# Kernel tuning notes

Hardware: AMD Instinct MI355X
Metric: run time of the kernel (lower is better)

## Reference

```python
import jax, jax.numpy as jnp
import numpy as np

N_NODES = 100000
N_EDGES = 1600000
N_GRAPHS = 256
HIDDEN = 128
IN_FEAT = 5


def setup_inputs() -> dict:
    key = jax.random.key(0)
    ks = jax.random.split(key, 12)
    x = jax.random.normal(ks[0], (N_NODES, IN_FEAT), dtype=jnp.float32)
    edge_index = jax.random.randint(ks[1], (2, N_EDGES), 0, N_NODES, dtype=jnp.int64)
    batch = jnp.sort(jax.random.randint(ks[2], (N_NODES,), 0, N_GRAPHS, dtype=jnp.int64))
    s = 0.05
    W0 = jax.random.normal(ks[3], (IN_FEAT, HIDDEN), dtype=jnp.float32) * s
    b0 = jnp.zeros((HIDDEN,), dtype=jnp.float32)
    W1 = jax.random.normal(ks[4], (HIDDEN, HIDDEN), dtype=jnp.float32) * s
    b1 = jnp.zeros((HIDDEN,), dtype=jnp.float32)
    W2 = jax.random.normal(ks[5], (HIDDEN, HIDDEN), dtype=jnp.float32) * s
    b2 = jnp.zeros((HIDDEN,), dtype=jnp.float32)
    lin_w = jax.random.normal(ks[6], (HIDDEN, 1), dtype=jnp.float32) * s
    lin_b = jnp.zeros((1,), dtype=jnp.float32)
    return {"x": x, "edge_index": edge_index, "batch": batch,
            "W0": W0, "b0": b0, "W1": W1, "b1": b1, "W2": W2, "b2": b2,
            "lin_w": lin_w, "lin_b": lin_b}


def reference(x, edge_index, batch, W0, b0, W1, b1, W2, b2, lin_w, lin_b):
    n = x.shape[0]
    # PyG GCNConv: add self-loops, symmetric normalization D^-1/2 (A+I) D^-1/2
    loop = jnp.arange(n, dtype=edge_index.dtype)
    src = jnp.concatenate([edge_index[0], loop])  # [E+N]
    dst = jnp.concatenate([edge_index[1], loop])
    deg = jax.ops.segment_sum(jnp.ones_like(dst, dtype=x.dtype), dst, num_segments=n)
    dis = jnp.where(deg > 0, jax.lax.rsqrt(jnp.maximum(deg, 1.0)), 0.0)
    norm = (dis[src] * dis[dst])[:, None]  # [E+N, 1]

    def gcn_conv(h, W, b):
        h = h @ W                      # [N, H]
        msg = h[src] * norm            # gather + scale, [E+N, H]
        return jax.ops.segment_sum(msg, dst, num_segments=n) + b

    h = jax.nn.relu(gcn_conv(x, W0, b0))
    h = jax.nn.relu(gcn_conv(h, W1, b1))
    h = gcn_conv(h, W2, b2)

    # global_mean_pool over batch ids
    sums = jax.ops.segment_sum(h, batch, num_segments=N_GRAPHS)
    cnt = jax.ops.segment_sum(jnp.ones((n,), x.dtype), batch, num_segments=N_GRAPHS)
    g = sums / jnp.maximum(cnt, 1.0)[:, None]
    # dropout p=0.01 is identity in eval mode
    return jax.nn.sigmoid(g @ lin_w + lin_b)  # [N_GRAPHS, 1]
```

## Files before the change

kernel.cpp:

```cpp
#include <hip/hip_runtime.h>
#include <hip/hip_fp8.h>

#define GCN_N 100000
#define GCN_H 128
#define GCN_G 256
#define NPB_SHIFT 9
#define NPB 512
#define NBKT 196
#define CHUNK 2048
#define SRC_BITS 17
#define SRC_MASK ((1 << SRC_BITS) - 1)
#define T1_SCALE 256.0f
#define T1_INV_SCALE (1.0f / 256.0f)

static_assert(GCN_N < (1 << SRC_BITS), "src id must fit 17 bits");

using short8 = __attribute__((ext_vector_type(8))) short;
using f32x4  = __attribute__((ext_vector_type(4))) float;
using f32x2  = __attribute__((ext_vector_type(2))) float;

#if defined(__has_builtin)
#if __has_builtin(__builtin_amdgcn_cvt_pk_f32_fp8) && __has_builtin(__builtin_amdgcn_cvt_pk_fp8_f32)
#define HW_FP8 1
#endif
#endif


__device__ __forceinline__ unsigned short f2bf(float f) {
    unsigned u = __float_as_uint(f);
    unsigned r = u + 0x7FFFu + ((u >> 16) & 1u);
    return (unsigned short)(r >> 16);
}
__device__ __forceinline__ float bf2f(unsigned short h) {
    return __uint_as_float(((unsigned)h) << 16);
}

__device__ __forceinline__ void fp8x4_to_f32(unsigned v, float* f) {
#ifdef HW_FP8
    f32x2 lo = __builtin_amdgcn_cvt_pk_f32_fp8((int)v, false);
    f32x2 hi = __builtin_amdgcn_cvt_pk_f32_fp8((int)v, true);
    f[0] = lo[0]; f[1] = lo[1]; f[2] = hi[0]; f[3] = hi[1];
#else
    #pragma unroll
    for (int j = 0; j < 4; j++) {
        __hip_fp8_e4m3 h;
        h.__x = (unsigned char)((v >> (8 * j)) & 0xFF);
        f[j] = (float)h;
    }
#endif
}

__device__ __forceinline__ unsigned f32x4_to_fp8(float f0, float f1, float f2, float f3) {
#ifdef HW_FP8
    int r = __builtin_amdgcn_cvt_pk_fp8_f32(f0, f1, 0, false);
    r = __builtin_amdgcn_cvt_pk_fp8_f32(f2, f3, r, true);
    return (unsigned)r;
#else
    unsigned r = 0;
    float ff[4] = {f0, f1, f2, f3};
    #pragma unroll
    for (int j = 0; j < 4; j++) {
        __hip_fp8_e4m3 h(ff[j]);
        r |= ((unsigned)h.__x) << (8 * j);
    }
    return r;
#endif
}


__global__ __launch_bounds__(256) void hist_kernel(const int* __restrict__ dst,
                                                   int* __restrict__ hist, int E) {
    __shared__ int lh[NBKT];
    int tid = threadIdx.x;
    if (tid < NBKT) lh[tid] = 0;
    __syncthreads();
    int e0 = blockIdx.x * CHUNK;
    #pragma unroll
    for (int i = 0; i < CHUNK / 256; i++) {
        int e = e0 + tid + i * 256;
        if (e < E) atomicAdd(&lh[dst[e] >> NPB_SHIFT], 1);
    }
    __syncthreads();
    if (tid < NBKT) hist[(size_t)blockIdx.x * NBKT + tid] = lh[tid];
}

__global__ __launch_bounds__(64) void scan_cols_kernel(const int* __restrict__ hist,
                                                       int* __restrict__ offsT,
                                                       int* __restrict__ btot, int B) {
    int k = blockIdx.x;
    int lane = threadIdx.x;
    int running = 0;
    for (int b0 = 0; b0 < B; b0 += 64) {
        int b = b0 + lane;
        int v = (b < B) ? hist[(size_t)b * NBKT + k] : 0;
        int iv = v;
        #pragma unroll
        for (int d = 1; d < 64; d <<= 1) {
            int x = __shfl_up(iv, d, 64);
            if (lane >= d) iv += x;
        }
        if (b < B) offsT[(size_t)k * B + b] = running + iv - v;
        running += __shfl(iv, 63, 64);
    }
    if (lane == 0) btot[k] = running;
}

__global__ void bucket_base_kernel(const int* __restrict__ btot,
                                   int* __restrict__ bbase,
                                   int* __restrict__ rowptr, int n) {
    if (threadIdx.x == 0 && blockIdx.x == 0) {
        int run = 0;
        for (int i = 0; i < NBKT; i++) { bbase[i] = run; run += btot[i]; }
        bbase[NBKT] = run;
        rowptr[n] = run;
    }
}

__global__ __launch_bounds__(256) void partition_kernel(const int* __restrict__ src,
                                                        const int* __restrict__ dst,
                                                        const int* __restrict__ bbase,
                                                        const int* __restrict__ offsT,
                                                        int* __restrict__ epack,
                                                        int E, int B) {
    __shared__ int cur[NBKT];
    int blk = blockIdx.x, tid = threadIdx.x;
    if (tid < NBKT) cur[tid] = bbase[tid] + offsT[(size_t)tid * B + blk];
    __syncthreads();
    int e0 = blk * CHUNK;
    #pragma unroll
    for (int i = 0; i < CHUNK / 256; i++) {
        int e = e0 + tid + i * 256;
        if (e < E) {
            int d = dst[e];
            int s = src[e];
            int pos = atomicAdd(&cur[d >> NPB_SHIFT], 1);
            epack[pos] = ((d & (NPB - 1)) << SRC_BITS) | s;
        }
    }
}

__global__ __launch_bounds__(512) void csr_build_kernel(const int* __restrict__ epack,
                                                        const int* __restrict__ bbase,
                                                        int* __restrict__ rowptr,
                                                        float* __restrict__ dis,
                                                        int* __restrict__ csrc, int n) {
    __shared__ int lcount[NPB];
    __shared__ int lcur[NPB];
    __shared__ int wsums[8];
    int k = blockIdx.x, tid = threadIdx.x;
    int lane = tid & 63, wid = tid >> 6;
    int nodebase = k << NPB_SHIFT;
    int ebeg = bbase[k], eend = bbase[k + 1];

    lcount[tid] = 0;
    __syncthreads();
    for (int e = ebeg + tid; e < eend; e += 512)
        atomicAdd(&lcount[epack[e] >> SRC_BITS], 1);
    __syncthreads();

    int v = lcount[tid];
    int iv = v;
    #pragma unroll
    for (int d = 1; d < 64; d <<= 1) {
        int x = __shfl_up(iv, d, 64);
        if (lane >= d) iv += x;
    }
    if (lane == 63) wsums[wid] = iv;
    __syncthreads();
    if (tid == 0) {
        int r = 0;
        #pragma unroll
        for (int w = 0; w < 8; w++) { int t = wsums[w]; wsums[w] = r; r += t; }
    }
    __syncthreads();
    int ex = wsums[wid] + iv - v;
    lcur[tid] = ex;
    int node = nodebase + tid;
    if (node < n) {
        rowptr[node] = ebeg + ex;
        dis[node] = rsqrtf((float)(v + 1));
    }
    __syncthreads();
    for (int e = ebeg + tid; e < eend; e += 512) {
        int p = epack[e];
        int pos = atomicAdd(&lcur[p >> SRC_BITS], 1);
        csrc[ebeg + pos] = p & SRC_MASK;
    }
}


__global__ __launch_bounds__(256) void xscale_kernel(const float* __restrict__ x,
                                                     const float* __restrict__ dis,
                                                     float* __restrict__ xsp, int n) {
    int i = blockIdx.x * 256 + threadIdx.x;
    if (i >= n) return;
    float di = dis[i];
    float4 a;
    a.x = x[(size_t)i * 5 + 0] * di;
    a.y = x[(size_t)i * 5 + 1] * di;
    a.z = x[(size_t)i * 5 + 2] * di;
    a.w = x[(size_t)i * 5 + 3] * di;
    float a4 = x[(size_t)i * 5 + 4] * di;
    ((float4*)(xsp + (size_t)i * 8))[0] = a;
    xsp[(size_t)i * 8 + 4] = a4;
}

__global__ __launch_bounds__(256) void aggx_kernel(const float* __restrict__ xsp,
                                                   const float* __restrict__ dis,
                                                   const int* __restrict__ rowptr,
                                                   const int* __restrict__ csrc,
                                                   float* __restrict__ a0p, int n) {
    int i = blockIdx.x * 256 + threadIdx.x;
    if (i >= n) return;
    float4 acc = ((const float4*)(xsp + (size_t)i * 8))[0];
    float acc4 = xsp[(size_t)i * 8 + 4];
    int r0 = rowptr[i], r1 = rowptr[i + 1];
    for (int e = r0; e < r1; e++) {
        int s = csrc[e];
        float4 v = ((const float4*)(xsp + (size_t)s * 8))[0];
        acc.x += v.x; acc.y += v.y; acc.z += v.z; acc.w += v.w;
        acc4 += xsp[(size_t)s * 8 + 4];
    }
    float di = dis[i];
    acc.x *= di; acc.y *= di; acc.z *= di; acc.w *= di; acc4 *= di;
    ((float4*)(a0p + (size_t)i * 8))[0] = acc;
    a0p[(size_t)i * 8 + 4] = acc4;
}


__global__ __launch_bounds__(256) void mmfused_kernel(const float* __restrict__ a0p,
                                                      const float* __restrict__ W0,
                                                      const float* __restrict__ b0,
                                                      const float* __restrict__ W1,
                                                      const float* __restrict__ dis,
                                                      unsigned* __restrict__ t1f8, int n) {
    __shared__ __align__(16) unsigned short sA[128 * 128];
    __shared__ __align__(16) unsigned short sBT[128 * 128];
    __shared__ __align__(16) float4 sA0[256];
    __shared__ float sDis[128];
    char* sAb = (char*)sA;
    char* sBb = (char*)sBT;
    int tid = threadIdx.x;
    int rowBase = blockIdx.x * 128;

    {
        int rowL = tid >> 1, q = tid & 1;
        int gr = rowBase + rowL;
        float4 v = make_float4(0.f, 0.f, 0.f, 0.f);
        if (gr < n) v = ((const float4*)a0p)[(size_t)gr * 2 + q];
        sA0[tid] = v;
        if (tid < 128) {
            int g2 = rowBase + tid;
            sDis[tid] = (g2 < n) ? dis[g2] : 0.f;
        }
    }
    for (int idx = tid; idx < 128 * 32; idx += 256) {
        int k = idx >> 5, c4 = idx & 31;
        float4 w = ((const float4*)W1)[idx];
        int col0 = c4 * 4;
        float wv[4] = {w.x, w.y, w.z, w.w};
        #pragma unroll
        for (int j = 0; j < 4; j++) {
            int col = col0 + j;
            int byteoff = (col * 256 + k * 2) ^ ((col & 7) << 4);
            *(unsigned short*)(sBb + byteoff) = f2bf(wv[j]);
        }
    }
    __syncthreads();

    {
        int cq = tid & 31;
        int rg = tid >> 5;
        float4 w0q[5];
        #pragma unroll
        for (int j = 0; j < 5; j++) w0q[j] = *((const float4*)(W0 + j * 128 + cq * 4));
        float4 b0q = *((const float4*)(b0 + cq * 4));
        const float* sA0f = (const float*)sA0;
        #pragma unroll
        for (int ri = 0; ri < 16; ri++) {
            int row = rg + ri * 8;
            const float* ar = sA0f + row * 8;
            float4 h = b0q;
            #pragma unroll
            for (int j = 0; j < 5; j++) {
                float aj = ar[j];
                h.x = fmaf(aj, w0q[j].x, h.x);
                h.y = fmaf(aj, w0q[j].y, h.y);
                h.z = fmaf(aj, w0q[j].z, h.z);
                h.w = fmaf(aj, w0q[j].w, h.w);
            }
            h.x = fmaxf(h.x, 0.f); h.y = fmaxf(h.y, 0.f);
            h.z = fmaxf(h.z, 0.f); h.w = fmaxf(h.w, 0.f);
            uint2 p;
            p.x = (unsigned)f2bf(h.x) | ((unsigned)f2bf(h.y) << 16);
            p.y = (unsigned)f2bf(h.z) | ((unsigned)f2bf(h.w) << 16);
            int byteoff = (row * 256 + cq * 8) ^ ((row & 7) << 4);
            *(uint2*)(sAb + byteoff) = p;
        }
    }
    __syncthreads();

    int wave = tid >> 6, l = tid & 63;
    int lr = l & 15, lg = l >> 4;
    int rb = wave * 32;

    short8 afr[2][4];
    #pragma unroll
    for (int rt = 0; rt < 2; rt++) {
        int row = rb + rt * 16 + lr;
        #pragma unroll
        for (int ks = 0; ks < 4; ks++) {
            int byteoff = (row * 256 + ks * 64 + lg * 16) ^ ((row & 7) << 4);
            afr[rt][ks] = *(const short8*)(sAb + byteoff);
        }
    }
    f32x4 acc[2][8];
    #pragma unroll
    for (int rt = 0; rt < 2; rt++)
        #pragma unroll
        for (int ct = 0; ct < 8; ct++)
            acc[rt][ct] = (f32x4){0.f, 0.f, 0.f, 0.f};

    #pragma unroll
    for (int ct = 0; ct < 8; ct++) {
        int col = ct * 16 + lr;
        short8 bfr[4];
        #pragma unroll
        for (int ks = 0; ks < 4; ks++) {
            int byteoff = (col * 256 + ks * 64 + lg * 16) ^ ((col & 7) << 4);
            bfr[ks] = *(const short8*)(sBb + byteoff);
        }
        #pragma unroll
        for (int rt = 0; rt < 2; rt++) {
            #pragma unroll
            for (int ks = 0; ks < 4; ks++) {
                acc[rt][ct] = __builtin_amdgcn_mfma_f32_16x16x32_bf16(
                    afr[rt][ks], bfr[ks], acc[rt][ct], 0, 0, 0);
            }
        }
    }

    #pragma unroll
    for (int rt = 0; rt < 2; rt++) {
        #pragma unroll
        for (int i = 0; i < 4; i++) {
            int rowL = rb + rt * 16 + lg * 4 + i;
            float dsc = sDis[rowL] * T1_SCALE;
            #pragma unroll
            for (int ct = 0; ct < 8; ct++) {
                int col = ct * 16 + lr;
                int byteoff = (rowL * 256 + col * 2) ^ ((rowL & 7) << 4);
                *(unsigned short*)(sAb + byteoff) = f2bf(acc[rt][ct][i] * dsc);
            }
        }
    }
    __syncthreads();

    #pragma unroll
    for (int it = 0; it < 8; it++) {
        int flat = tid + it * 256;
        int rowL = flat >> 4, c16 = flat & 15;
        int gr = rowBase + rowL;
        if (gr < n) {
            int byteoff = (rowL * 256 + c16 * 16) ^ ((rowL & 7) << 4);
            uint4 v = *(const uint4*)(sAb + byteoff);
            float f0 = __uint_as_float(v.x << 16), f1 = __uint_as_float(v.x & 0xFFFF0000u);
            float f2 = __uint_as_float(v.y << 16), f3 = __uint_as_float(v.y & 0xFFFF0000u);
            float f4 = __uint_as_float(v.z << 16), f5 = __uint_as_float(v.z & 0xFFFF0000u);
            float f6 = __uint_as_float(v.w << 16), f7 = __uint_as_float(v.w & 0xFFFF0000u);
            uint2 p;
            p.x = f32x4_to_fp8(f0, f1, f2, f3);
            p.y = f32x4_to_fp8(f4, f5, f6, f7);
            ((uint2*)t1f8)[(size_t)gr * 16 + c16] = p;
        }
    }
}


__global__ __launch_bounds__(256) void w2l_kernel(const float* __restrict__ W2,
                                                  const float* __restrict__ b2,
                                                  const float* __restrict__ lw,
                                                  float* __restrict__ w2l,
                                                  float* __restrict__ c2) {
    __shared__ float slw[128];
    int tid = threadIdx.x;
    if (tid < 128) slw[tid] = lw[tid];
    __syncthreads();
    if (tid < 128) {
        float s = 0.f;
        #pragma unroll 8
        for (int j = 0; j < 128; j++) s = fmaf(W2[tid * 128 + j], slw[j], s);
        w2l[tid] = s;
    } else if (tid == 128) {
        float s = 0.f;
        for (int j = 0; j < 128; j++) s = fmaf(b2[j], slw[j], s);
        c2[0] = s;
    }
}


__global__ __launch_bounds__(256) void agg1_kernel(const unsigned* __restrict__ t1f8,
                                                   const float* __restrict__ dis,
                                                   const int* __restrict__ rowptr,
                                                   const int* __restrict__ csrc,
                                                   const float* __restrict__ b1,
                                                   const float* __restrict__ w2l,
                                                   float* __restrict__ z, int n) {
    int group = threadIdx.x >> 5, lane = threadIdx.x & 31;
    int i = blockIdx.x * 8 + group;
    if (i >= n) return;
    float f[4];
    unsigned sv = t1f8[(size_t)i * 32 + lane];
    fp8x4_to_f32(sv, f);
    float4 acc = make_float4(f[0], f[1], f[2], f[3]);
    int r0 = rowptr[i], r1 = rowptr[i + 1];
    int e = r0;
    for (; e + 7 < r1; e += 8) {
        unsigned vv[8];
        #pragma unroll
        for (int u = 0; u < 8; u++) vv[u] = t1f8[(size_t)csrc[e + u] * 32 + lane];
        #pragma unroll
        for (int u = 0; u < 8; u++) {
            fp8x4_to_f32(vv[u], f);
            acc.x += f[0]; acc.y += f[1]; acc.z += f[2]; acc.w += f[3];
        }
    }
    for (; e < r1; e++) {
        unsigned v = t1f8[(size_t)csrc[e] * 32 + lane];
        fp8x4_to_f32(v, f);
        acc.x += f[0]; acc.y += f[1]; acc.z += f[2]; acc.w += f[3];
    }
    float di = dis[i];
    float dis_s = di * T1_INV_SCALE;
    float4 b4 = ((const float4*)b1)[lane];
    acc.x = fmaf(dis_s, acc.x, b4.x);
    acc.y = fmaf(dis_s, acc.y, b4.y);
    acc.z = fmaf(dis_s, acc.z, b4.z);
    acc.w = fmaf(dis_s, acc.w, b4.w);
    acc.x = fmaxf(acc.x, 0.f); acc.y = fmaxf(acc.y, 0.f);
    acc.z = fmaxf(acc.z, 0.f); acc.w = fmaxf(acc.w, 0.f);
    float4 w = ((const float4*)w2l)[lane];
    float d = acc.x * w.x + acc.y * w.y + acc.z * w.z + acc.w * w.w;
    #pragma unroll
    for (int o = 16; o > 0; o >>= 1) d += __shfl_down(d, o, 32);
    if (lane == 0) z[i] = di * d;
}


__global__ __launch_bounds__(256) void aggz_kernel(const float* __restrict__ z,
                                                   const float* __restrict__ dis,
                                                   const int* __restrict__ rowptr,
                                                   const int* __restrict__ csrc,
                                                   float* __restrict__ nd, int n) {
    int i = blockIdx.x * 256 + threadIdx.x;
    if (i >= n) return;
    float acc = z[i];
    int r0 = rowptr[i], r1 = rowptr[i + 1];
    int e = r0;
    for (; e + 3 < r1; e += 4) {
        acc += (z[csrc[e]] + z[csrc[e + 1]]) + (z[csrc[e + 2]] + z[csrc[e + 3]]);
    }
    for (; e < r1; e++) acc += z[csrc[e]];
    nd[i] = dis[i] * acc;
}


__global__ __launch_bounds__(256) void boundary_kernel(const int* __restrict__ batch,
                                                       int* __restrict__ gstart, int n) {
    int i = blockIdx.x * 256 + threadIdx.x;
    if (i >= n) return;
    int b = batch[i];
    int pb = (i == 0) ? -1 : batch[i - 1];
    for (int g = pb + 1; g <= b; g++) gstart[g] = i;
    if (i == n - 1) {
        for (int g = b + 1; g <= GCN_G; g++) gstart[g] = n;
    }
}

__global__ __launch_bounds__(256) void reduce_kernel(const float* __restrict__ nd,
                                                     const int* __restrict__ gstart,
                                                     const float* __restrict__ c2,
                                                     const float* __restrict__ lb,
                                                     float* __restrict__ out) {
    __shared__ float ssum[4];
    int g = blockIdx.x;
    int s = gstart[g], epos = gstart[g + 1];
    int tid = threadIdx.x, lane = tid & 63, wid = tid >> 6;
    float sum = 0.f;
    for (int i = s + tid; i < epos; i += 256) sum += nd[i];
    #pragma unroll
    for (int o = 32; o > 0; o >>= 1) sum += __shfl_down(sum, o, 64);
    if (lane == 0) ssum[wid] = sum;
    __syncthreads();
    if (tid == 0) {
        float tot = ssum[0] + ssum[1] + ssum[2] + ssum[3];
        float cnt = (float)max(epos - s, 1);
        float v = tot / cnt + c2[0] + lb[0];
        out[g] = 1.f / (1.f + expf(-v));
    }
}


extern "C" void kernel_launch(void* const* d_in, const int* in_sizes, int n_in,
                              void* d_out, int out_size, void* d_ws, size_t ws_size,
                              hipStream_t stream) {
    const float* x   = (const float*)d_in[0];
    const int*   ei  = (const int*)d_in[1];
    const int*   bat = (const int*)d_in[2];
    const float* W0  = (const float*)d_in[3];
    const float* b0  = (const float*)d_in[4];
    const float* W1  = (const float*)d_in[5];
    const float* b1  = (const float*)d_in[6];
    const float* W2  = (const float*)d_in[7];
    const float* b2  = (const float*)d_in[8];
    const float* lw  = (const float*)d_in[9];
    const float* lb  = (const float*)d_in[10];
    float* out = (float*)d_out;

    const int N = GCN_N;
    const int E = in_sizes[1] / 2;
    const int B = (E + CHUNK - 1) / CHUNK;

    char* ws = (char*)d_ws;
    size_t off = 0;
    auto alloc = [&](size_t bytes) {
        size_t o = off;
        off += (bytes + 255) & ~(size_t)255;
        return o;
    };
    int*   hist    = (int*)(ws + alloc((size_t)B * NBKT * 4));
    int*   offsT   = (int*)(ws + alloc((size_t)NBKT * B * 4));
    int*   btot    = (int*)(ws + alloc((size_t)NBKT * 4));
    int*   bbase   = (int*)(ws + alloc((size_t)(NBKT + 1) * 4));
    int*   epack   = (int*)(ws + alloc((size_t)E * 4));
    int*   rowptr  = (int*)(ws + alloc((size_t)(N + 1) * 4));
    float* dis     = (float*)(ws + alloc((size_t)N * 4));
    int*   csrc    = (int*)(ws + alloc((size_t)E * 4));
    float* xsp     = (float*)(ws + alloc((size_t)N * 8 * 4));
    float* a0p     = (float*)(ws + alloc((size_t)N * 8 * 4));
    unsigned* t1f8 = (unsigned*)(ws + alloc((size_t)N * GCN_H));
    float* z       = (float*)(ws + alloc((size_t)N * 4));
    float* nd      = (float*)(ws + alloc((size_t)N * 4));
    int*   gstart  = (int*)(ws + alloc((size_t)(GCN_G + 1) * 4));
    float* w2l     = (float*)(ws + alloc(128 * 4));
    float* c2      = (float*)(ws + alloc(4));

    const int* src = ei;
    const int* dst = ei + E;

    hist_kernel<<<B, 256, 0, stream>>>(dst, hist, E);
    scan_cols_kernel<<<NBKT, 64, 0, stream>>>(hist, offsT, btot, B);
    bucket_base_kernel<<<1, 64, 0, stream>>>(btot, bbase, rowptr, N);
    partition_kernel<<<B, 256, 0, stream>>>(src, dst, bbase, offsT, epack, E, B);
    csr_build_kernel<<<NBKT, 512, 0, stream>>>(epack, bbase, rowptr, dis, csrc, N);
    boundary_kernel<<<(N + 255) / 256, 256, 0, stream>>>(bat, gstart, N);
    w2l_kernel<<<1, 256, 0, stream>>>(W2, b2, lw, w2l, c2);

    xscale_kernel<<<(N + 255) / 256, 256, 0, stream>>>(x, dis, xsp, N);
    aggx_kernel<<<(N + 255) / 256, 256, 0, stream>>>(xsp, dis, rowptr, csrc, a0p, N);
    mmfused_kernel<<<(N + 127) / 128, 256, 0, stream>>>(a0p, W0, b0, W1, dis, t1f8, N);
    agg1_kernel<<<N / 8, 256, 0, stream>>>(t1f8, dis, rowptr, csrc, b1, w2l, z, N);
    aggz_kernel<<<(N + 255) / 256, 256, 0, stream>>>(z, dis, rowptr, csrc, nd, N);

    reduce_kernel<<<GCN_G, 256, 0, stream>>>(nd, gstart, c2, lb, out);
}
```

Baseline: 170.8 us.

## Fuse x scaling into CSR build, pre-convert W1, fuse pooling into final aggregation

Several independent changes. The x-scaling kernel is folded into the CSR build, and W1 is converted to transposed bf16 once in a small kernel so each matmul block does vector loads instead of per-element conversion. The first aggregation is unrolled by four. agg1 now gives each node 16 lanes of 8 fp8 values each, so each block covers twice as many nodes. The last aggregation is fused with mean pooling through shared-memory and global atomics, which removes the nd buffer and the per-graph reduce kernel but adds a memset and float atomic ordering nondeterminism.

New measurement: 152.0 us. 11.0% less time.

```diff
diff --git a/kernel.cpp b/kernel.cpp
--- a/kernel.cpp
+++ b/kernel.cpp
@@ -141,8 +141,10 @@
 
 __global__ __launch_bounds__(512) void csr_build_kernel(const int* __restrict__ epack,
                                                         const int* __restrict__ bbase,
+                                                        const float* __restrict__ x,
                                                         int* __restrict__ rowptr,
                                                         float* __restrict__ dis,
+                                                        float* __restrict__ xsp,
                                                         int* __restrict__ csrc, int n) {
     __shared__ int lcount[NPB];
     __shared__ int lcur[NPB];
@@ -162,8 +164,8 @@
     int iv = v;
     #pragma unroll
     for (int d = 1; d < 64; d <<= 1) {
-        int x = __shfl_up(iv, d, 64);
-        if (lane >= d) iv += x;
+        int x2 = __shfl_up(iv, d, 64);
+        if (lane >= d) iv += x2;
     }
     if (lane == 63) wsums[wid] = iv;
     __syncthreads();
@@ -178,7 +180,17 @@
     int node = nodebase + tid;
     if (node < n) {
         rowptr[node] = ebeg + ex;
-        dis[node] = rsqrtf((float)(v + 1));
+        float dd = rsqrtf((float)(v + 1));
+        dis[node] = dd;
+        const float* xr = x + (size_t)node * 5;
+        float4 a;
+        a.x = xr[0] * dd; a.y = xr[1] * dd; a.z = xr[2] * dd; a.w = xr[3] * dd;
+        float a4 = xr[4] * dd;
+        ((float4*)(xsp + (size_t)node * 8))[0] = a;
+        xsp[(size_t)node * 8 + 4] = a4;
+        xsp[(size_t)node * 8 + 5] = 0.f;
+        xsp[(size_t)node * 8 + 6] = 0.f;
+        xsp[(size_t)node * 8 + 7] = 0.f;
     }
     __syncthreads();
     for (int e = ebeg + tid; e < eend; e += 512) {
@@ -188,22 +200,6 @@
     }
 }
 
-
-__global__ __launch_bounds__(256) void xscale_kernel(const float* __restrict__ x,
-                                                     const float* __restrict__ dis,
-                                                     float* __restrict__ xsp, int n) {
-    int i = blockIdx.x * 256 + threadIdx.x;
-    if (i >= n) return;
-    float di = dis[i];
-    float4 a;
-    a.x = x[(size_t)i * 5 + 0] * di;
-    a.y = x[(size_t)i * 5 + 1] * di;
-    a.z = x[(size_t)i * 5 + 2] * di;
-    a.w = x[(size_t)i * 5 + 3] * di;
-    float a4 = x[(size_t)i * 5 + 4] * di;
-    ((float4*)(xsp + (size_t)i * 8))[0] = a;
-    xsp[(size_t)i * 8 + 4] = a4;
-}
 
 __global__ __launch_bounds__(256) void aggx_kernel(const float* __restrict__ xsp,
                                                    const float* __restrict__ dis,
@@ -215,7 +211,24 @@
     float4 acc = ((const float4*)(xsp + (size_t)i * 8))[0];
     float acc4 = xsp[(size_t)i * 8 + 4];
     int r0 = rowptr[i], r1 = rowptr[i + 1];
-    for (int e = r0; e < r1; e++) {
+    int e = r0;
+    for (; e + 3 < r1; e += 4) {
+        int s0 = csrc[e], s1 = csrc[e + 1], s2 = csrc[e + 2], s3 = csrc[e + 3];
+        float4 v0 = ((const float4*)(xsp + (size_t)s0 * 8))[0];
+        float a40 = xsp[(size_t)s0 * 8 + 4];
+        float4 v1 = ((const float4*)(xsp + (size_t)s1 * 8))[0];
+        float a41 = xsp[(size_t)s1 * 8 + 4];
+        float4 v2 = ((const float4*)(xsp + (size_t)s2 * 8))[0];
+        float a42 = xsp[(size_t)s2 * 8 + 4];
+        float4 v3 = ((const float4*)(xsp + (size_t)s3 * 8))[0];
+        float a43 = xsp[(size_t)s3 * 8 + 4];
+        acc.x += (v0.x + v1.x) + (v2.x + v3.x);
+        acc.y += (v0.y + v1.y) + (v2.y + v3.y);
+        acc.z += (v0.z + v1.z) + (v2.z + v3.z);
+        acc.w += (v0.w + v1.w) + (v2.w + v3.w);
+        acc4  += (a40 + a41) + (a42 + a43);
+    }
+    for (; e < r1; e++) {
         int s = csrc[e];
         float4 v = ((const float4*)(xsp + (size_t)s * 8))[0];
         acc.x += v.x; acc.y += v.y; acc.z += v.z; acc.w += v.w;
@@ -228,10 +241,39 @@
 }
 
 
+__global__ __launch_bounds__(256) void w2l_kernel(const float* __restrict__ W2,
+                                                  const float* __restrict__ b2,
+                                                  const float* __restrict__ lw,
+                                                  float* __restrict__ w2l,
+                                                  float* __restrict__ c2) {
+    __shared__ float slw[128];
+    int tid = threadIdx.x;
+    if (tid < 128) slw[tid] = lw[tid];
+    __syncthreads();
+    if (tid < 128) {
+        float s = 0.f;
+        #pragma unroll 8
+        for (int j = 0; j < 128; j++) s = fmaf(W2[tid * 128 + j], slw[j], s);
+        w2l[tid] = s;
+    } else if (tid == 128) {
+        float s = 0.f;
+        for (int j = 0; j < 128; j++) s = fmaf(b2[j], slw[j], s);
+        c2[0] = s;
+    }
+}
+
+__global__ __launch_bounds__(256) void w1cvt_kernel(const float* __restrict__ W1,
+                                                    unsigned short* __restrict__ w1t) {
+    int idx = blockIdx.x * 256 + threadIdx.x;
+    int col = idx >> 7, k = idx & 127;
+    w1t[idx] = f2bf(W1[k * 128 + col]);
+}
+
+
 __global__ __launch_bounds__(256) void mmfused_kernel(const float* __restrict__ a0p,
                                                       const float* __restrict__ W0,
                                                       const float* __restrict__ b0,
-                                                      const float* __restrict__ W1,
+                                                      const unsigned short* __restrict__ w1t,
                                                       const float* __restrict__ dis,
                                                       unsigned* __restrict__ t1f8, int n) {
     __shared__ __align__(16) unsigned short sA[128 * 128];
@@ -254,17 +296,13 @@
             sDis[tid] = (g2 < n) ? dis[g2] : 0.f;
         }
     }
-    for (int idx = tid; idx < 128 * 32; idx += 256) {
-        int k = idx >> 5, c4 = idx & 31;
-        float4 w = ((const float4*)W1)[idx];
-        int col0 = c4 * 4;
-        float wv[4] = {w.x, w.y, w.z, w.w};
-        #pragma unroll
-        for (int j = 0; j < 4; j++) {
-            int col = col0 + j;
-            int byteoff = (col * 256 + k * 2) ^ ((col & 7) << 4);
-            *(unsigned short*)(sBb + byteoff) = f2bf(wv[j]);
-        }
+    #pragma unroll
+    for (int it = 0; it < 8; it++) {
+        int idx = tid + it * 256;
+        int col = idx >> 4, c = idx & 15;
+        uint4 v = ((const uint4*)w1t)[idx];
+        int byteoff = (col * 256 + c * 16) ^ ((col & 7) << 4);
+        *(uint4*)(sBb + byteoff) = v;
     }
     __syncthreads();
 
@@ -377,28 +415,6 @@
 }
 
 
-__global__ __launch_bounds__(256) void w2l_kernel(const float* __restrict__ W2,
-                                                  const float* __restrict__ b2,
-                                                  const float* __restrict__ lw,
-                                                  float* __restrict__ w2l,
-                                                  float* __restrict__ c2) {
-    __shared__ float slw[128];
-    int tid = threadIdx.x;
-    if (tid < 128) slw[tid] = lw[tid];
-    __syncthreads();
-    if (tid < 128) {
-        float s = 0.f;
-        #pragma unroll 8
-        for (int j = 0; j < 128; j++) s = fmaf(W2[tid * 128 + j], slw[j], s);
-        w2l[tid] = s;
-    } else if (tid == 128) {
-        float s = 0.f;
-        for (int j = 0; j < 128; j++) s = fmaf(b2[j], slw[j], s);
-        c2[0] = s;
-    }
-}
-
-
 __global__ __launch_bounds__(256) void agg1_kernel(const unsigned* __restrict__ t1f8,
                                                    const float* __restrict__ dis,
                                                    const int* __restrict__ rowptr,
@@ -406,62 +422,96 @@
                                                    const float* __restrict__ b1,
                                                    const float* __restrict__ w2l,
                                                    float* __restrict__ z, int n) {
-    int group = threadIdx.x >> 5, lane = threadIdx.x & 31;
-    int i = blockIdx.x * 8 + group;
+    int group = threadIdx.x >> 4, lane = threadIdx.x & 15;
+    int i = blockIdx.x * 16 + group;
     if (i >= n) return;
-    float f[4];
-    unsigned sv = t1f8[(size_t)i * 32 + lane];
-    fp8x4_to_f32(sv, f);
-    float4 acc = make_float4(f[0], f[1], f[2], f[3]);
+    const uint2* t2 = (const uint2*)t1f8;
+    float f[8];
+    uint2 sv = t2[(size_t)i * 16 + lane];
+    fp8x4_to_f32(sv.x, f);
+    fp8x4_to_f32(sv.y, f + 4);
+    float acc[8];
+    #pragma unroll
+    for (int j = 0; j < 8; j++) acc[j] = f[j];
     int r0 = rowptr[i], r1 = rowptr[i + 1];
     int e = r0;
     for (; e + 7 < r1; e += 8) {
-        unsigned vv[8];
-        #pragma unroll
-        for (int u = 0; u < 8; u++) vv[u] = t1f8[(size_t)csrc[e + u] * 32 + lane];
+        uint2 vv[8];
+        #pragma unroll
+        for (int u = 0; u < 8; u++) vv[u] = t2[(size_t)csrc[e + u] * 16 + lane];
         #pragma unroll
         for (int u = 0; u < 8; u++) {
-            fp8x4_to_f32(vv[u], f);
-            acc.x += f[0]; acc.y += f[1]; acc.z += f[2]; acc.w += f[3];
+            fp8x4_to_f32(vv[u].x, f);
+            fp8x4_to_f32(vv[u].y, f + 4);
+            #pragma unroll
+            for (int j = 0; j < 8; j++) acc[j] += f[j];
         }
     }
     for (; e < r1; e++) {
-        unsigned v = t1f8[(size_t)csrc[e] * 32 + lane];
-        fp8x4_to_f32(v, f);
-        acc.x += f[0]; acc.y += f[1]; acc.z += f[2]; acc.w += f[3];
+        uint2 v = t2[(size_t)csrc[e] * 16 + lane];
+        fp8x4_to_f32(v.x, f);
+        fp8x4_to_f32(v.y, f + 4);
+        #pragma unroll
+        for (int j = 0; j < 8; j++) acc[j] += f[j];
     }
     float di = dis[i];
     float dis_s = di * T1_INV_SCALE;
-    float4 b4 = ((const float4*)b1)[lane];
-    acc.x = fmaf(dis_s, acc.x, b4.x);
-    acc.y = fmaf(dis_s, acc.y, b4.y);
-    acc.z = fmaf(dis_s, acc.z, b4.z);
-    acc.w = fmaf(dis_s, acc.w, b4.w);
-    acc.x = fmaxf(acc.x, 0.f); acc.y = fmaxf(acc.y, 0.f);
-    acc.z = fmaxf(acc.z, 0.f); acc.w = fmaxf(acc.w, 0.f);
-    float4 w = ((const float4*)w2l)[lane];
-    float d = acc.x * w.x + acc.y * w.y + acc.z * w.z + acc.w * w.w;
-    #pragma unroll
-    for (int o = 16; o > 0; o >>= 1) d += __shfl_down(d, o, 32);
+    float4 b4a = ((const float4*)b1)[lane * 2];
+    float4 b4b = ((const float4*)b1)[lane * 2 + 1];
+    float4 w4a = ((const float4*)w2l)[lane * 2];
+    float4 w4b = ((const float4*)w2l)[lane * 2 + 1];
+    float bb[8] = {b4a.x, b4a.y, b4a.z, b4a.w, b4b.x, b4b.y, b4b.z, b4b.w};
+    float ww[8] = {w4a.x, w4a.y, w4a.z, w4a.w, w4b.x, w4b.y, w4b.z, w4b.w};
+    float d = 0.f;
+    #pragma unroll
+    for (int j = 0; j < 8; j++) {
+        float c = fmaxf(fmaf(dis_s, acc[j], bb[j]), 0.f);
+        d = fmaf(c, ww[j], d);
+    }
+    #pragma unroll
+    for (int o = 8; o > 0; o >>= 1) d += __shfl_down(d, o, 16);
     if (lane == 0) z[i] = di * d;
 }
 
 
-__global__ __launch_bounds__(256) void aggz_kernel(const float* __restrict__ z,
-                                                   const float* __restrict__ dis,
-                                                   const int* __restrict__ rowptr,
-                                                   const int* __restrict__ csrc,
-                                                   float* __restrict__ nd, int n) {
-    int i = blockIdx.x * 256 + threadIdx.x;
-    if (i >= n) return;
-    float acc = z[i];
-    int r0 = rowptr[i], r1 = rowptr[i + 1];
-    int e = r0;
-    for (; e + 3 < r1; e += 4) {
-        acc += (z[csrc[e]] + z[csrc[e + 1]]) + (z[csrc[e + 2]] + z[csrc[e + 3]]);
-    }
-    for (; e < r1; e++) acc += z[csrc[e]];
-    nd[i] = dis[i] * acc;
+__global__ __launch_bounds__(256) void aggz_pool_kernel(const float* __restrict__ z,
+                                                        const float* __restrict__ dis,
+                                                        const int* __restrict__ rowptr,
+                                                        const int* __restrict__ csrc,
+                                                        const int* __restrict__ batch,
+                                                        float* __restrict__ gsum, int n) {
+    __shared__ float lg[GCN_G];
+    int tid = threadIdx.x;
+    lg[tid] = 0.f;
+    __syncthreads();
+    int i = blockIdx.x * 256 + tid;
+    float ndv = 0.f;
+    int g = 0;
+    if (i < n) {
+        float acc = z[i];
+        int r0 = rowptr[i], r1 = rowptr[i + 1];
+        int e = r0;
+        for (; e + 3 < r1; e += 4) {
+            acc += (z[csrc[e]] + z[csrc[e + 1]]) + (z[csrc[e + 2]] + z[csrc[e + 3]]);
+        }
+        for (; e < r1; e++) acc += z[csrc[e]];
+        ndv = dis[i] * acc;
+        g = batch[i];
+    }
+    int lane = tid & 63;
+    int g0 = __shfl(g, 0, 64);
+    bool uni = __all(g == g0);
+    if (uni) {
+        float s = ndv;
+        #pragma unroll
+        for (int o = 32; o > 0; o >>= 1) s += __shfl_down(s, o, 64);
+        if (lane == 0 && s != 0.f) atomicAdd(&lg[g0], s);
+    } else {
+        if (ndv != 0.f) atomicAdd(&lg[g], ndv);
+    }
+    __syncthreads();
+    float v = lg[tid];
+    if (v != 0.f) atomicAdd(&gsum[tid], v);
 }
 
 
@@ -477,27 +527,15 @@
     }
 }
 
-__global__ __launch_bounds__(256) void reduce_kernel(const float* __restrict__ nd,
-                                                     const int* __restrict__ gstart,
-                                                     const float* __restrict__ c2,
-                                                     const float* __restrict__ lb,
-                                                     float* __restrict__ out) {
-    __shared__ float ssum[4];
-    int g = blockIdx.x;
-    int s = gstart[g], epos = gstart[g + 1];
-    int tid = threadIdx.x, lane = tid & 63, wid = tid >> 6;
-    float sum = 0.f;
-    for (int i = s + tid; i < epos; i += 256) sum += nd[i];
-    #pragma unroll
-    for (int o = 32; o > 0; o >>= 1) sum += __shfl_down(sum, o, 64);
-    if (lane == 0) ssum[wid] = sum;
-    __syncthreads();
-    if (tid == 0) {
-        float tot = ssum[0] + ssum[1] + ssum[2] + ssum[3];
-        float cnt = (float)max(epos - s, 1);
-        float v = tot / cnt + c2[0] + lb[0];
-        out[g] = 1.f / (1.f + expf(-v));
-    }
+__global__ __launch_bounds__(256) void final_kernel(const float* __restrict__ gsum,
+                                                    const int* __restrict__ gstart,
+                                                    const float* __restrict__ c2,
+                                                    const float* __restrict__ lb,
+                                                    float* __restrict__ out) {
+    int g = threadIdx.x;
+    float cnt = (float)max(gstart[g + 1] - gstart[g], 1);
+    float v = gsum[g] / cnt + c2[0] + lb[0];
+    out[g] = 1.f / (1.f + expf(-v));
 }
 
 
@@ -540,27 +578,30 @@
     float* a0p     = (float*)(ws + alloc((size_t)N * 8 * 4));
     unsigned* t1f8 = (unsigned*)(ws + alloc((size_t)N * GCN_H));
     float* z       = (float*)(ws + alloc((size_t)N * 4));
-    float* nd      = (float*)(ws + alloc((size_t)N * 4));
     int*   gstart  = (int*)(ws + alloc((size_t)(GCN_G + 1) * 4));
     float* w2l     = (float*)(ws + alloc(128 * 4));
     float* c2      = (float*)(ws + alloc(4));
+    unsigned short* w1t = (unsigned short*)(ws + alloc(128 * 128 * 2));
+    float* gsum    = (float*)(ws + alloc(GCN_G * 4));
 
     const int* src = ei;
     const int* dst = ei + E;
+
+    hipMemsetAsync(gsum, 0, GCN_G * 4, stream);
 
     hist_kernel<<<B, 256, 0, stream>>>(dst, hist, E);
     scan_cols_kernel<<<NBKT, 64, 0, stream>>>(hist, offsT, btot, B);
     bucket_base_kernel<<<1, 64, 0, stream>>>(btot, bbase, rowptr, N);
     partition_kernel<<<B, 256, 0, stream>>>(src, dst, bbase, offsT, epack, E, B);
-    csr_build_kernel<<<NBKT, 512, 0, stream>>>(epack, bbase, rowptr, dis, csrc, N);
+    csr_build_kernel<<<NBKT, 512, 0, stream>>>(epack, bbase, x, rowptr, dis, xsp, csrc, N);
     boundary_kernel<<<(N + 255) / 256, 256, 0, stream>>>(bat, gstart, N);
     w2l_kernel<<<1, 256, 0, stream>>>(W2, b2, lw, w2l, c2);
-
-    xscale_kernel<<<(N + 255) / 256, 256, 0, stream>>>(x, dis, xsp, N);
+    w1cvt_kernel<<<64, 256, 0, stream>>>(W1, w1t);
+
     aggx_kernel<<<(N + 255) / 256, 256, 0, stream>>>(xsp, dis, rowptr, csrc, a0p, N);
-    mmfused_kernel<<<(N + 127) / 128, 256, 0, stream>>>(a0p, W0, b0, W1, dis, t1f8, N);
-    agg1_kernel<<<N / 8, 256, 0, stream>>>(t1f8, dis, rowptr, csrc, b1, w2l, z, N);
-    aggz_kernel<<<(N + 255) / 256, 256, 0, stream>>>(z, dis, rowptr, csrc, nd, N);
-
-    reduce_kernel<<<GCN_G, 256, 0, stream>>>(nd, gstart, c2, lb, out);
-}
+    mmfused_kernel<<<(N + 127) / 128, 256, 0, stream>>>(a0p, W0, b0, w1t, dis, t1f8, N);
+    agg1_kernel<<<(N + 15) / 16, 256, 0, stream>>>(t1f8, dis, rowptr, csrc, b1, w2l, z, N);
+    aggz_pool_kernel<<<(N + 255) / 256, 256, 0, stream>>>(z, dis, rowptr, csrc, bat, gsum, N);
+
+    final_kernel<<<1, 256, 0, stream>>>(gsum, gstart, c2, lb, out);
+}
```
